# Performance work log

Hardware: AMD Instinct MI355X
Metric: run time of the kernel (lower is better)

## Reference

```python
import jax, jax.numpy as jnp
import numpy as np

EPS = 1e-12
BETA = 0.25

def normalise(x, axis=-1):
    return x * jax.lax.rsqrt(jnp.mean(x * x, axis=axis, keepdims=True) + EPS)

def setup_inputs() -> dict:
    key = jax.random.key(0)
    ks = jax.random.split(key, 4)
    N, F, D, C = 8192, 512, 64, 8192
    return {
        "z": jax.random.normal(ks[0], (N, F), dtype=jnp.float32),
        "W_in": jax.random.normal(ks[1], (F, D), dtype=jnp.float32) * (1.0 / np.sqrt(F)),
        "b_in": jnp.zeros((D,), dtype=jnp.float32),
        "codebook": jax.random.normal(ks[2], (C, D), dtype=jnp.float32),
        "W_out": jax.random.normal(ks[3], (D, F), dtype=jnp.float32) * (1.0 / np.sqrt(D)),
        "b_out": jnp.zeros((F,), dtype=jnp.float32),
    }

def reference(z, W_in, b_in, codebook, W_out, b_out):
    sg = jax.lax.stop_gradient
    # input projection: [N, F] -> [N, D]
    zp = z @ W_in + b_in
    zn = normalise(zp)                  # [N, D]
    cn = normalise(codebook)            # [C, D]
    # squared euclidean distance via matmul expansion (same math as
    # sum((z[:,None]-c[None])**2, -1), avoids [N,C,D] materialization)
    z_sq = jnp.sum(zn * zn, axis=-1, keepdims=True)          # [N, 1]
    c_sq = jnp.sum(cn * cn, axis=-1)[None, :]                # [1, C]
    distance = z_sq + c_sq - 2.0 * (zn @ cn.T)               # [N, C]
    idxes = jnp.argmin(distance, axis=-1)                    # [N]
    codes = normalise(codebook[idxes], axis=-1)               # [N, D]
    loss = BETA * jnp.mean((sg(zn) - codes) ** 2) + jnp.mean((zn - sg(codes)) ** 2)
    codes = zn + sg(codes - zn)                               # straight-through
    out = codes @ W_out + b_out                               # [N, F]
    return (out, loss, idxes)
```

## Files before the change

kernel.cpp:

```cpp
#include <hip/hip_runtime.h>
#include <hip/hip_bf16.h>

#define N_ROWS 8192
#define F_DIM  512
#define D_DIM  64
#define C_CODES 8192

typedef __attribute__((ext_vector_type(8))) short bf16x8;
typedef __attribute__((ext_vector_type(4))) float f32x4;

__device__ __forceinline__ unsigned short rne_bf16(float x) {
  unsigned u = __float_as_uint(x);
  return (unsigned short)((u + 0x7FFFu + ((u >> 16) & 1u)) >> 16);
}
__device__ __forceinline__ float bf16_to_f(unsigned short u) {
  return __uint_as_float(((unsigned)u) << 16);
}
__device__ __forceinline__ void limb3(const float* xs, bf16x8& H, bf16x8& M, bf16x8& L) {
  #pragma unroll
  for (int j = 0; j < 8; ++j) {
    float x = xs[j];
    unsigned short h = rne_bf16(x);
    float r1 = x - bf16_to_f(h);
    unsigned short m = rne_bf16(r1);
    float r2 = r1 - bf16_to_f(m);
    unsigned short lo = rne_bf16(r2);
    H[j] = (short)h; M[j] = (short)m; L[j] = (short)lo;
  }
}

typedef __attribute__((address_space(1))) const unsigned char gas_uchar;
typedef __attribute__((address_space(3))) unsigned char las_uchar;
__device__ __forceinline__ void gld_lds16(const void* g, void* l) {
  __builtin_amdgcn_global_load_lds((gas_uchar*)g, (las_uchar*)l, 16, 0, 0);
}

__global__ __launch_bounds__(256) void k_prep(
    const float* __restrict__ W_in, const float* __restrict__ W_out,
    const float* __restrict__ cb,
    unsigned short* __restrict__ win_sw, unsigned short* __restrict__ wout_sw,
    float* __restrict__ cn, unsigned short* __restrict__ cn_sw) {
  const int tid = threadIdx.x, w = tid >> 6, l = tid & 63;
  const int lo = l & 15, hi = l >> 4;
  const int bid = blockIdx.x;

  if (bid < 16) {
    const int task = bid * 4 + w;
    const int kc = task >> 2, cg = task & 3;
    float xs[8];
    #pragma unroll
    for (int j = 0; j < 8; ++j)
      xs[j] = W_in[(size_t)(kc * 32 + hi * 8 + j) * D_DIM + cg * 16 + lo];
    bf16x8 H, M, L;
    limb3(xs, H, M, L);
    const int fb = (kc * 4 + cg) * 3;
    unsigned short* d0 = win_sw + (size_t)(fb + 0) * 512 + l * 8;
    unsigned short* d1 = win_sw + (size_t)(fb + 1) * 512 + l * 8;
    unsigned short* d2 = win_sw + (size_t)(fb + 2) * 512 + l * 8;
    #pragma unroll
    for (int j = 0; j < 8; ++j) { d0[j] = (unsigned short)H[j]; d1[j] = (unsigned short)M[j]; d2[j] = (unsigned short)L[j]; }
  } else if (bid < 32) {
    const int task = (bid - 16) * 4 + w;
    const int cg = task >> 1, c = task & 1;
    float xs[8];
    #pragma unroll
    for (int j = 0; j < 8; ++j)
      xs[j] = W_out[(size_t)(c * 32 + hi * 8 + j) * F_DIM + cg * 16 + lo];
    bf16x8 H, M, L;
    limb3(xs, H, M, L);
    const int fb = (cg * 2 + c) * 3;
    unsigned short* d0 = wout_sw + (size_t)(fb + 0) * 512 + l * 8;
    unsigned short* d1 = wout_sw + (size_t)(fb + 1) * 512 + l * 8;
    unsigned short* d2 = wout_sw + (size_t)(fb + 2) * 512 + l * 8;
    #pragma unroll
    for (int j = 0; j < 8; ++j) { d0[j] = (unsigned short)H[j]; d1[j] = (unsigned short)M[j]; d2[j] = (unsigned short)L[j]; }
  } else {
    const int g = (bid - 32) * 4 + w;
    const int code = g * 16 + lo;
    float xs[2][8];
    float s = 0.0f;
    #pragma unroll
    for (int c = 0; c < 2; ++c) {
      const float* sp = cb + (size_t)code * D_DIM + c * 32 + hi * 8;
      float4 a = *(const float4*)sp, b = *(const float4*)(sp + 4);
      xs[c][0]=a.x; xs[c][1]=a.y; xs[c][2]=a.z; xs[c][3]=a.w;
      xs[c][4]=b.x; xs[c][5]=b.y; xs[c][6]=b.z; xs[c][7]=b.w;
      #pragma unroll
      for (int j = 0; j < 8; ++j) s += xs[c][j] * xs[c][j];
    }
    s += __shfl_xor(s, 16);
    s += __shfl_xor(s, 32);
    float inv = rsqrtf(s * (1.0f / 64.0f) + 1e-12f);
    #pragma unroll
    for (int c = 0; c < 2; ++c) {
      #pragma unroll
      for (int j = 0; j < 8; ++j) xs[c][j] *= inv;
      float* dp = cn + (size_t)code * D_DIM + c * 32 + hi * 8;
      *(float4*)dp = make_float4(xs[c][0], xs[c][1], xs[c][2], xs[c][3]);
      *(float4*)(dp + 4) = make_float4(xs[c][4], xs[c][5], xs[c][6], xs[c][7]);
      bf16x8 H, M, L;
      limb3(xs[c], H, M, L);
      const int fb = (g * 2 + c) * 3;
      unsigned short* d0 = cn_sw + (size_t)(fb + 0) * 512 + l * 8;
      unsigned short* d1 = cn_sw + (size_t)(fb + 1) * 512 + l * 8;
      unsigned short* d2 = cn_sw + (size_t)(fb + 2) * 512 + l * 8;
      #pragma unroll
      for (int j = 0; j < 8; ++j) { d0[j] = (unsigned short)H[j]; d1[j] = (unsigned short)M[j]; d2[j] = (unsigned short)L[j]; }
    }
  }
}

__global__ __launch_bounds__(256) void k_zn(
    const float* __restrict__ z, const unsigned short* __restrict__ w_in_sw,
    const float* __restrict__ b_in, float* __restrict__ zn,
    unsigned short* __restrict__ zn_sw) {
  __shared__ float red[4096];
  __shared__ float t_lds[16 * 65];
  const int tid = threadIdx.x, w = tid >> 6, l = tid & 63;
  const int lo = l & 15, hi = l >> 4;
  const int g = blockIdx.x;
  const int r0 = g * 16;
  const int kcb = w * 4;
  const bf16x8* Bptr = (const bf16x8*)w_in_sw;
  const float* zbase = z + (size_t)(r0 + lo) * F_DIM + hi * 8;

  f32x4 acc[4];
  #pragma unroll
  for (int cg = 0; cg < 4; ++cg) acc[cg] = (f32x4){0.f, 0.f, 0.f, 0.f};

  bf16x8 Bu[12], Bv[12];
  #pragma unroll
  for (int i = 0; i < 12; ++i) Bu[i] = Bptr[((size_t)kcb * 12 + i) * 64 + l];
  float4 za = *(const float4*)(zbase + kcb * 32);
  float4 zb = *(const float4*)(zbase + kcb * 32 + 4);

  #define ZMFMA(BCUR)                                                         \
    {                                                                         \
      float xs[8] = {za.x, za.y, za.z, za.w, zb.x, zb.y, zb.z, zb.w};         \
      bf16x8 Ah, Am, Al;                                                      \
      limb3(xs, Ah, Am, Al);                                                  \
      _Pragma("unroll")                                                       \
      for (int cg = 0; cg < 4; ++cg) {                                        \
        f32x4 t = acc[cg];                                                    \
        t = __builtin_amdgcn_mfma_f32_16x16x32_bf16(Ah, BCUR[cg*3+0], t, 0,0,0); \
        t = __builtin_amdgcn_mfma_f32_16x16x32_bf16(Ah, BCUR[cg*3+1], t, 0,0,0); \
        t = __builtin_amdgcn_mfma_f32_16x16x32_bf16(Am, BCUR[cg*3+0], t, 0,0,0); \
        t = __builtin_amdgcn_mfma_f32_16x16x32_bf16(Ah, BCUR[cg*3+2], t, 0,0,0); \
        t = __builtin_amdgcn_mfma_f32_16x16x32_bf16(Al, BCUR[cg*3+0], t, 0,0,0); \
        t = __builtin_amdgcn_mfma_f32_16x16x32_bf16(Am, BCUR[cg*3+1], t, 0,0,0); \
        acc[cg] = t;                                                          \
      }                                                                       \
    }

  {
    float4 na = *(const float4*)(zbase + (kcb + 1) * 32);
    float4 nb = *(const float4*)(zbase + (kcb + 1) * 32 + 4);
    #pragma unroll
    for (int i = 0; i < 12; ++i) Bv[i] = Bptr[((size_t)(kcb + 1) * 12 + i) * 64 + l];
    ZMFMA(Bu)
    za = na; zb = nb;
  }
  {
    float4 na = *(const float4*)(zbase + (kcb + 2) * 32);
    float4 nb = *(const float4*)(zbase + (kcb + 2) * 32 + 4);
    #pragma unroll
    for (int i = 0; i < 12; ++i) Bu[i] = Bptr[((size_t)(kcb + 2) * 12 + i) * 64 + l];
    ZMFMA(Bv)
    za = na; zb = nb;
  }
  {
    float4 na = *(const float4*)(zbase + (kcb + 3) * 32);
    float4 nb = *(const float4*)(zbase + (kcb + 3) * 32 + 4);
    #pragma unroll
    for (int i = 0; i < 12; ++i) Bv[i] = Bptr[((size_t)(kcb + 3) * 12 + i) * 64 + l];
    ZMFMA(Bu)
    za = na; zb = nb;
  }
  ZMFMA(Bv)
  #undef ZMFMA

  #pragma unroll
  for (int cg = 0; cg < 4; ++cg)
    #pragma unroll
    for (int r = 0; r < 4; ++r)
      red[((w * 4 + cg) * 4 + r) * 64 + l] = acc[cg][r];
  __syncthreads();

  {
    float v[4], s = 0.0f;
    #pragma unroll
    for (int cg = 0; cg < 4; ++cg) {
      float t = b_in[cg * 16 + lo];
      #pragma unroll
      for (int w2 = 0; w2 < 4; ++w2) t += red[((w2 * 4 + cg) * 4 + w) * 64 + l];
      v[cg] = t; s += t * t;
    }
    s += __shfl_xor(s, 1);
    s += __shfl_xor(s, 2);
    s += __shfl_xor(s, 4);
    s += __shfl_xor(s, 8);
    float inv = rsqrtf(s * (1.0f / 64.0f) + 1e-12f);
    #pragma unroll
    for (int cg = 0; cg < 4; ++cg)
      t_lds[(hi * 4 + w) * 65 + cg * 16 + lo] = v[cg] * inv;
  }
  __syncthreads();

  if (w < 2) {
    const int c = w;
    float xs[8];
    #pragma unroll
    for (int j = 0; j < 8; ++j) xs[j] = t_lds[lo * 65 + c * 32 + hi * 8 + j];
    float* dp = zn + (size_t)(r0 + lo) * D_DIM + c * 32 + hi * 8;
    *(float4*)dp = make_float4(xs[0], xs[1], xs[2], xs[3]);
    *(float4*)(dp + 4) = make_float4(xs[4], xs[5], xs[6], xs[7]);
    bf16x8 H, M, L;
    limb3(xs, H, M, L);
    const int fb = (g * 2 + c) * 3;
    unsigned short* d0 = zn_sw + (size_t)(fb + 0) * 512 + l * 8;
    unsigned short* d1 = zn_sw + (size_t)(fb + 1) * 512 + l * 8;
    unsigned short* d2 = zn_sw + (size_t)(fb + 2) * 512 + l * 8;
    #pragma unroll
    for (int j = 0; j < 8; ++j) { d0[j] = (unsigned short)H[j]; d1[j] = (unsigned short)M[j]; d2[j] = (unsigned short)L[j]; }
  }
}

__global__ __launch_bounds__(256) void k_argmax(
    const unsigned short* __restrict__ zn_sw,
    const unsigned short* __restrict__ cn_sw,
    float* __restrict__ pval, int* __restrict__ pidx) {
  __shared__ short smem[2 * 12 * 512];
  const int tid = threadIdx.x;
  const int w = tid >> 6, l = tid & 63;
  const int lo = l & 15, hi = l >> 4;
  const int gA0 = (blockIdx.x * 4 + w) * 2;
  const int gB0 = blockIdx.y * 32;
  const bf16x8* Ab = (const bf16x8*)zn_sw;
  const char* Bbytes = (const char*)cn_sw;

  bf16x8 A0[2][3], A1[2][3];
  #pragma unroll
  for (int c = 0; c < 2; ++c)
    #pragma unroll
    for (int m = 0; m < 3; ++m) {
      A0[c][m] = Ab[(size_t)((gA0 * 2 + c) * 3 + m) * 64 + l];
      A1[c][m] = Ab[(size_t)(((gA0 + 1) * 2 + c) * 3 + m) * 64 + l];
    }

  float bv[8];
  int bi[8];
  #pragma unroll
  for (int i = 0; i < 8; ++i) { bv[i] = -1e30f; bi[i] = 0; }
  int cand = blockIdx.y * 512 + lo;

  #define STAGE(b, s)                                                         \
    {                                                                         \
      const int fb = (gB0 + (s) * 2) * 6 + w * 3;                             \
      _Pragma("unroll")                                                       \
      for (int i = 0; i < 3; ++i)                                             \
        gld_lds16(Bbytes + ((size_t)(fb + i) << 10) + (size_t)l * 16,         \
                  &smem[((b) * 12 + w * 3 + i) * 512]);                       \
    }

  #define MF(A_, B_, C_) __builtin_amdgcn_mfma_f32_16x16x32_bf16(A_, B_, C_, 0, 0, 0)

  #define COMPUTE(LF)                                                         \
    {                                                                         \
      bf16x8 Bf[6];                                                           \
      _Pragma("unroll")                                                       \
      for (int i = 0; i < 6; ++i)                                             \
        Bf[i] = *(const bf16x8*)&smem[((LF) + i) * 512 + l * 8];              \
      f32x4 a0 = {0.f,0.f,0.f,0.f}, a1 = {0.f,0.f,0.f,0.f};                   \
      f32x4 a2 = {0.f,0.f,0.f,0.f}, a3 = {0.f,0.f,0.f,0.f};                   \
      a0 = MF(A0[0][0], Bf[0], a0); a1 = MF(A0[1][0], Bf[3], a1);             \
      a2 = MF(A1[0][0], Bf[0], a2); a3 = MF(A1[1][0], Bf[3], a3);             \
      a0 = MF(A0[0][0], Bf[1], a0); a1 = MF(A0[1][0], Bf[4], a1);             \
      a2 = MF(A1[0][0], Bf[1], a2); a3 = MF(A1[1][0], Bf[4], a3);             \
      a0 = MF(A0[0][1], Bf[0], a0); a1 = MF(A0[1][1], Bf[3], a1);             \
      a2 = MF(A1[0][1], Bf[0], a2); a3 = MF(A1[1][1], Bf[3], a3);             \
      a0 = MF(A0[0][0], Bf[2], a0); a1 = MF(A0[1][0], Bf[5], a1);             \
      a2 = MF(A1[0][0], Bf[2], a2); a3 = MF(A1[1][0], Bf[5], a3);             \
      a0 = MF(A0[0][2], Bf[0], a0); a1 = MF(A0[1][2], Bf[3], a1);             \
      a2 = MF(A1[0][2], Bf[0], a2); a3 = MF(A1[1][2], Bf[3], a3);             \
      a0 = MF(A0[0][1], Bf[1], a0); a1 = MF(A0[1][1], Bf[4], a1);             \
      a2 = MF(A1[0][1], Bf[1], a2); a3 = MF(A1[1][1], Bf[4], a3);             \
      _Pragma("unroll")                                                       \
      for (int r = 0; r < 4; ++r) {                                           \
        float d0 = a0[r] + a1[r];                                             \
        if (d0 > bv[r]) { bv[r] = d0; bi[r] = cand; }                         \
        float d1 = a2[r] + a3[r];                                             \
        if (d1 > bv[4 + r]) { bv[4 + r] = d1; bi[4 + r] = cand; }             \
      }                                                                       \
      cand += 16;                                                             \
    }

  STAGE(0, 0)
  __syncthreads();
  int cur = 0;
  for (int s = 0; s < 16; ++s) {
    if (s < 15) STAGE(cur ^ 1, s + 1)
    COMPUTE(cur * 12 + 0)
    COMPUTE(cur * 12 + 6)
    __syncthreads();
    cur ^= 1;
  }
  #undef STAGE
  #undef COMPUTE
  #undef MF

  #pragma unroll
  for (int i = 0; i < 8; ++i) {
    float v = bv[i]; int ix = bi[i];
    #pragma unroll
    for (int m = 1; m < 16; m <<= 1) {
      float ov = __shfl_xor(v, m);
      int oi = __shfl_xor(ix, m);
      if (ov > v || (ov == v && oi < ix)) { v = ov; ix = oi; }
    }
    bv[i] = v; bi[i] = ix;
  }
  if (lo == 0) {
    int off = blockIdx.y * N_ROWS;
    int base0 = gA0 * 16 + hi * 4;
    int base1 = (gA0 + 1) * 16 + hi * 4;
    #pragma unroll
    for (int r = 0; r < 4; ++r) {
      pval[off + base0 + r] = bv[r];     pidx[off + base0 + r] = bi[r];
      pval[off + base1 + r] = bv[4 + r]; pidx[off + base1 + r] = bi[4 + r];
    }
  }
}

__global__ __launch_bounds__(256) void k_out(
    const float* __restrict__ cn, const float* __restrict__ zn,
    const float* __restrict__ pval, const int* __restrict__ pidx,
    const unsigned short* __restrict__ w_out_sw,
    const float* __restrict__ b_out, float* __restrict__ out,
    float* __restrict__ idx_f, float* __restrict__ pl) {
  const int tid = threadIdx.x, w = tid >> 6, l = tid & 63;
  const int lo = l & 15, hi = l >> 4;
  const int r0 = blockIdx.x * 16;
  const int row = r0 + lo;

  float v = pval[row];
  int ix = pidx[row];
  #pragma unroll
  for (int q = 1; q < 16; ++q) {
    float vq = pval[q * N_ROWS + row];
    int iq = pidx[q * N_ROWS + row];
    if (vq > v) { v = vq; ix = iq; }
  }
  if (w == 0 && hi == 0) idx_f[row] = (float)ix;

  bf16x8 A[2][3];
  float lp = 0.0f;
  #pragma unroll
  for (int c = 0; c < 2; ++c) {
    const float* cp = cn + (size_t)ix * D_DIM + c * 32 + hi * 8;
    const float* zp = zn + (size_t)row * D_DIM + c * 32 + hi * 8;
    float4 c0 = *(const float4*)cp, c1 = *(const float4*)(cp + 4);
    float4 z0 = *(const float4*)zp, z1 = *(const float4*)(zp + 4);
    float xs[8] = {c0.x, c0.y, c0.z, c0.w, c1.x, c1.y, c1.z, c1.w};
    float zs[8] = {z0.x, z0.y, z0.z, z0.w, z1.x, z1.y, z1.z, z1.w};
    limb3(xs, A[c][0], A[c][1], A[c][2]);
    #pragma unroll
    for (int j = 0; j < 8; ++j) { float d = xs[j] - zs[j]; lp += d * d; }
  }
  if (w == 0) {
    #pragma unroll
    for (int m = 1; m < 64; m <<= 1) lp += __shfl_xor(lp, m);
    if (l == 0) pl[blockIdx.x] = lp;
  }

  const bf16x8* Bptr = (const bf16x8*)w_out_sw;
  const int cgb = w * 8;
  bf16x8 Bu[6], Bv[6];
  #pragma unroll
  for (int i = 0; i < 6; ++i) Bu[i] = Bptr[((size_t)cgb * 6 + i) * 64 + l];

  #define OSTEP(BCUR, BNXT, CG)                                               \
    {                                                                         \
      _Pragma("unroll")                                                       \
      for (int i = 0; i < 6; ++i)                                             \
        BNXT[i] = Bptr[((size_t)((CG) + 1) * 6 + i) * 64 + l];                \
      f32x4 a0 = {0.f,0.f,0.f,0.f}, a1 = {0.f,0.f,0.f,0.f};                   \
      a0 = __builtin_amdgcn_mfma_f32_16x16x32_bf16(A[0][0], BCUR[0], a0, 0,0,0); \
      a1 = __builtin_amdgcn_mfma_f32_16x16x32_bf16(A[1][0], BCUR[3], a1, 0,0,0); \
      a0 = __builtin_amdgcn_mfma_f32_16x16x32_bf16(A[0][0], BCUR[1], a0, 0,0,0); \
      a1 = __builtin_amdgcn_mfma_f32_16x16x32_bf16(A[1][0], BCUR[4], a1, 0,0,0); \
      a0 = __builtin_amdgcn_mfma_f32_16x16x32_bf16(A[0][1], BCUR[0], a0, 0,0,0); \
      a1 = __builtin_amdgcn_mfma_f32_16x16x32_bf16(A[1][1], BCUR[3], a1, 0,0,0); \
      a0 = __builtin_amdgcn_mfma_f32_16x16x32_bf16(A[0][0], BCUR[2], a0, 0,0,0); \
      a1 = __builtin_amdgcn_mfma_f32_16x16x32_bf16(A[1][0], BCUR[5], a1, 0,0,0); \
      a0 = __builtin_amdgcn_mfma_f32_16x16x32_bf16(A[0][2], BCUR[0], a0, 0,0,0); \
      a1 = __builtin_amdgcn_mfma_f32_16x16x32_bf16(A[1][2], BCUR[3], a1, 0,0,0); \
      a0 = __builtin_amdgcn_mfma_f32_16x16x32_bf16(A[0][1], BCUR[1], a0, 0,0,0); \
      a1 = __builtin_amdgcn_mfma_f32_16x16x32_bf16(A[1][1], BCUR[4], a1, 0,0,0); \
      float bb = b_out[(CG) * 16 + lo];                                       \
      _Pragma("unroll")                                                       \
      for (int r = 0; r < 4; ++r)                                             \
        out[(size_t)(r0 + hi * 4 + r) * F_DIM + (CG) * 16 + lo] =             \
            a0[r] + a1[r] + bb;                                               \
    }

  for (int cg = cgb; cg < cgb + 8; cg += 2) {
    OSTEP(Bu, Bv, cg)
    OSTEP(Bv, Bu, cg + 1)
  }
  #undef OSTEP
}

__global__ __launch_bounds__(64) void k_loss_final(
    const float* __restrict__ pl, float* __restrict__ loss_out) {
  const int l = threadIdx.x;
  float s = 0.0f;
  #pragma unroll
  for (int i = 0; i < 8; ++i) s += pl[l + 64 * i];
  #pragma unroll
  for (int m = 1; m < 64; m <<= 1) s += __shfl_xor(s, m);
  if (l == 0) loss_out[0] = s * (1.25f / (float)(N_ROWS * D_DIM));
}

extern "C" void kernel_launch(void* const* d_in, const int* in_sizes, int n_in,
                              void* d_out, int out_size, void* d_ws, size_t ws_size,
                              hipStream_t stream) {
  const float* z        = (const float*)d_in[0];
  const float* W_in     = (const float*)d_in[1];
  const float* b_in     = (const float*)d_in[2];
  const float* codebook = (const float*)d_in[3];
  const float* W_out    = (const float*)d_in[4];
  const float* b_out    = (const float*)d_in[5];

  float* outp   = (float*)d_out;
  float* loss_f = outp + (size_t)N_ROWS * F_DIM;
  float* idx_f  = loss_f + 1;

  float* wsf = (float*)d_ws;
  float* zn_ws = wsf;
  float* cn_ws = wsf + 524288;
  unsigned short* zn_sw = (unsigned short*)(wsf + 1048576);
  unsigned short* cn_sw = (unsigned short*)(wsf + 1835008);
  unsigned short* win_sw  = (unsigned short*)(wsf + 2625536);
  unsigned short* wout_sw = (unsigned short*)(wsf + 2674688);
  float* pval_ws = wsf + 2723840;
  int*   pidx_ws = (int*)(wsf + 2854912);
  float* pl_ws   = wsf + 2985984;

  hipLaunchKernelGGL(k_prep, dim3(160), dim3(256), 0, stream,
                     W_in, W_out, codebook, win_sw, wout_sw, cn_ws, cn_sw);
  hipLaunchKernelGGL(k_zn, dim3(512), dim3(256), 0, stream,
                     z, win_sw, b_in, zn_ws, zn_sw);
  hipLaunchKernelGGL(k_argmax, dim3(64, 16), dim3(256), 0, stream,
                     zn_sw, cn_sw, pval_ws, pidx_ws);
  hipLaunchKernelGGL(k_out, dim3(512), dim3(256), 0, stream,
                     cn_ws, zn_ws, pval_ws, pidx_ws, wout_sw, b_out,
                     outp, idx_f, pl_ws);
  hipLaunchKernelGGL(k_loss_final, dim3(1), dim3(64), 0, stream,
                     pl_ws, loss_f);
}
```

Before: 141.6 us.

## Switch argmax GEMM to 32x32x16 MFMA with matching swizzled operand layout

```diff
diff --git a/kernel.cpp b/kernel.cpp
--- a/kernel.cpp
+++ b/kernel.cpp
@@ -8,6 +8,7 @@
 
 typedef __attribute__((ext_vector_type(8))) short bf16x8;
 typedef __attribute__((ext_vector_type(4))) float f32x4;
+typedef __attribute__((ext_vector_type(16))) float f32x16;
 
 __device__ __forceinline__ unsigned short rne_bf16(float x) {
   unsigned u = __float_as_uint(x);
@@ -55,10 +56,9 @@
     limb3(xs, H, M, L);
     const int fb = (kc * 4 + cg) * 3;
     unsigned short* d0 = win_sw + (size_t)(fb + 0) * 512 + l * 8;
-    unsigned short* d1 = win_sw + (size_t)(fb + 1) * 512 + l * 8;
-    unsigned short* d2 = win_sw + (size_t)(fb + 2) * 512 + l * 8;
-    #pragma unroll
-    for (int j = 0; j < 8; ++j) { d0[j] = (unsigned short)H[j]; d1[j] = (unsigned short)M[j]; d2[j] = (unsigned short)L[j]; }
+    *(bf16x8*)d0 = H;
+    *(bf16x8*)(d0 + 512) = M;
+    *(bf16x8*)(d0 + 1024) = L;
   } else if (bid < 32) {
     const int task = (bid - 16) * 4 + w;
     const int cg = task >> 1, c = task & 1;
@@ -70,13 +70,13 @@
     limb3(xs, H, M, L);
     const int fb = (cg * 2 + c) * 3;
     unsigned short* d0 = wout_sw + (size_t)(fb + 0) * 512 + l * 8;
-    unsigned short* d1 = wout_sw + (size_t)(fb + 1) * 512 + l * 8;
-    unsigned short* d2 = wout_sw + (size_t)(fb + 2) * 512 + l * 8;
-    #pragma unroll
-    for (int j = 0; j < 8; ++j) { d0[j] = (unsigned short)H[j]; d1[j] = (unsigned short)M[j]; d2[j] = (unsigned short)L[j]; }
+    *(bf16x8*)d0 = H;
+    *(bf16x8*)(d0 + 512) = M;
+    *(bf16x8*)(d0 + 1024) = L;
   } else {
     const int g = (bid - 32) * 4 + w;
     const int code = g * 16 + lo;
+    const int Gc = g >> 1, hgc = g & 1;
     float xs[2][8];
     float s = 0.0f;
     #pragma unroll
@@ -100,12 +100,13 @@
       *(float4*)(dp + 4) = make_float4(xs[c][4], xs[c][5], xs[c][6], xs[c][7]);
       bf16x8 H, M, L;
       limb3(xs[c], H, M, L);
-      const int fb = (g * 2 + c) * 3;
-      unsigned short* d0 = cn_sw + (size_t)(fb + 0) * 512 + l * 8;
-      unsigned short* d1 = cn_sw + (size_t)(fb + 1) * 512 + l * 8;
-      unsigned short* d2 = cn_sw + (size_t)(fb + 2) * 512 + l * 8;
-      #pragma unroll
-      for (int j = 0; j < 8; ++j) { d0[j] = (unsigned short)H[j]; d1[j] = (unsigned short)M[j]; d2[j] = (unsigned short)L[j]; }
+      const int kc = c * 2 + (hi >> 1);
+      const int lane = hgc * 16 + lo + 32 * (hi & 1);
+      unsigned short* d0 =
+          cn_sw + ((size_t)Gc * 4 + kc) * 3 * 512 + (size_t)lane * 8;
+      *(bf16x8*)d0 = H;
+      *(bf16x8*)(d0 + 512) = M;
+      *(bf16x8*)(d0 + 1024) = L;
     }
   }
 }
@@ -206,22 +207,25 @@
   }
   __syncthreads();
 
-  if (w < 2) {
-    const int c = w;
+  if (l < 32) {
+    const int r = l & 15, kh = l >> 4;
+    const int kc = w;
     float xs[8];
     #pragma unroll
-    for (int j = 0; j < 8; ++j) xs[j] = t_lds[lo * 65 + c * 32 + hi * 8 + j];
-    float* dp = zn + (size_t)(r0 + lo) * D_DIM + c * 32 + hi * 8;
+    for (int j = 0; j < 8; ++j)
+      xs[j] = t_lds[r * 65 + kc * 16 + kh * 8 + j];
+    float* dp = zn + (size_t)(r0 + r) * D_DIM + kc * 16 + kh * 8;
     *(float4*)dp = make_float4(xs[0], xs[1], xs[2], xs[3]);
     *(float4*)(dp + 4) = make_float4(xs[4], xs[5], xs[6], xs[7]);
     bf16x8 H, M, L;
     limb3(xs, H, M, L);
-    const int fb = (g * 2 + c) * 3;
-    unsigned short* d0 = zn_sw + (size_t)(fb + 0) * 512 + l * 8;
-    unsigned short* d1 = zn_sw + (size_t)(fb + 1) * 512 + l * 8;
-    unsigned short* d2 = zn_sw + (size_t)(fb + 2) * 512 + l * 8;
-    #pragma unroll
-    for (int j = 0; j < 8; ++j) { d0[j] = (unsigned short)H[j]; d1[j] = (unsigned short)M[j]; d2[j] = (unsigned short)L[j]; }
+    const int G = g >> 1, hg = g & 1;
+    const int lane = hg * 16 + r + 32 * kh;
+    unsigned short* d0 =
+        zn_sw + ((size_t)G * 4 + kc) * 3 * 512 + (size_t)lane * 8;
+    *(bf16x8*)d0 = H;
+    *(bf16x8*)(d0 + 512) = M;
+    *(bf16x8*)(d0 + 1024) = L;
   }
 }
 
@@ -232,66 +236,53 @@
   __shared__ short smem[2 * 12 * 512];
   const int tid = threadIdx.x;
   const int w = tid >> 6, l = tid & 63;
-  const int lo = l & 15, hi = l >> 4;
-  const int gA0 = (blockIdx.x * 4 + w) * 2;
-  const int gB0 = blockIdx.y * 32;
+  const int G = blockIdx.x * 4 + w;
+  const int gB0 = blockIdx.y * 16;
   const bf16x8* Ab = (const bf16x8*)zn_sw;
   const char* Bbytes = (const char*)cn_sw;
 
-  bf16x8 A0[2][3], A1[2][3];
-  #pragma unroll
-  for (int c = 0; c < 2; ++c)
-    #pragma unroll
-    for (int m = 0; m < 3; ++m) {
-      A0[c][m] = Ab[(size_t)((gA0 * 2 + c) * 3 + m) * 64 + l];
-      A1[c][m] = Ab[(size_t)(((gA0 + 1) * 2 + c) * 3 + m) * 64 + l];
-    }
-
-  float bv[8];
-  int bi[8];
-  #pragma unroll
-  for (int i = 0; i < 8; ++i) { bv[i] = -1e30f; bi[i] = 0; }
-  int cand = blockIdx.y * 512 + lo;
-
-  #define STAGE(b, s)                                                         \
-    {                                                                         \
-      const int fb = (gB0 + (s) * 2) * 6 + w * 3;                             \
-      _Pragma("unroll")                                                       \
-      for (int i = 0; i < 3; ++i)                                             \
-        gld_lds16(Bbytes + ((size_t)(fb + i) << 10) + (size_t)l * 16,         \
-                  &smem[((b) * 12 + w * 3 + i) * 512]);                       \
-    }
-
-  #define MF(A_, B_, C_) __builtin_amdgcn_mfma_f32_16x16x32_bf16(A_, B_, C_, 0, 0, 0)
-
-  #define COMPUTE(LF)                                                         \
-    {                                                                         \
-      bf16x8 Bf[6];                                                           \
-      _Pragma("unroll")                                                       \
-      for (int i = 0; i < 6; ++i)                                             \
-        Bf[i] = *(const bf16x8*)&smem[((LF) + i) * 512 + l * 8];              \
-      f32x4 a0 = {0.f,0.f,0.f,0.f}, a1 = {0.f,0.f,0.f,0.f};                   \
-      f32x4 a2 = {0.f,0.f,0.f,0.f}, a3 = {0.f,0.f,0.f,0.f};                   \
-      a0 = MF(A0[0][0], Bf[0], a0); a1 = MF(A0[1][0], Bf[3], a1);             \
-      a2 = MF(A1[0][0], Bf[0], a2); a3 = MF(A1[1][0], Bf[3], a3);             \
-      a0 = MF(A0[0][0], Bf[1], a0); a1 = MF(A0[1][0], Bf[4], a1);             \
-      a2 = MF(A1[0][0], Bf[1], a2); a3 = MF(A1[1][0], Bf[4], a3);             \
-      a0 = MF(A0[0][1], Bf[0], a0); a1 = MF(A0[1][1], Bf[3], a1);             \
-      a2 = MF(A1[0][1], Bf[0], a2); a3 = MF(A1[1][1], Bf[3], a3);             \
-      a0 = MF(A0[0][0], Bf[2], a0); a1 = MF(A0[1][0], Bf[5], a1);             \
-      a2 = MF(A1[0][0], Bf[2], a2); a3 = MF(A1[1][0], Bf[5], a3);             \
-      a0 = MF(A0[0][2], Bf[0], a0); a1 = MF(A0[1][2], Bf[3], a1);             \
-      a2 = MF(A1[0][2], Bf[0], a2); a3 = MF(A1[1][2], Bf[3], a3);             \
-      a0 = MF(A0[0][1], Bf[1], a0); a1 = MF(A0[1][1], Bf[4], a1);             \
-      a2 = MF(A1[0][1], Bf[1], a2); a3 = MF(A1[1][1], Bf[4], a3);             \
-      _Pragma("unroll")                                                       \
-      for (int r = 0; r < 4; ++r) {                                           \
-        float d0 = a0[r] + a1[r];                                             \
-        if (d0 > bv[r]) { bv[r] = d0; bi[r] = cand; }                         \
-        float d1 = a2[r] + a3[r];                                             \
-        if (d1 > bv[4 + r]) { bv[4 + r] = d1; bi[4 + r] = cand; }             \
-      }                                                                       \
-      cand += 16;                                                             \
+  bf16x8 A[4][3];
+  #pragma unroll
+  for (int kc = 0; kc < 4; ++kc)
+    #pragma unroll
+    for (int m = 0; m < 3; ++m)
+      A[kc][m] = Ab[((size_t)(G * 4 + kc) * 3 + m) * 64 + l];
+
+  float bv[16];
+  int bi[16];
+  #pragma unroll
+  for (int i = 0; i < 16; ++i) { bv[i] = -1e30f; bi[i] = 0; }
+
+  #define STAGE(b, s)                                                        \
+    {                                                                        \
+      const int fb = (gB0 + (s)) * 12 + w * 3;                               \
+      _Pragma("unroll")                                                      \
+      for (int i = 0; i < 3; ++i)                                            \
+        gld_lds16(Bbytes + ((size_t)(fb + i) << 10) + (size_t)l * 16,        \
+                  &smem[((b) * 12 + w * 3 + i) * 512]);                      \
+    }
+
+  #define MF32(A_, B_, C_) __builtin_amdgcn_mfma_f32_32x32x16_bf16(A_, B_, C_, 0, 0, 0)
+
+  #define COMPUTE(LF, s)                                                     \
+    {                                                                        \
+      f32x16 acc = {};                                                       \
+      _Pragma("unroll")                                                      \
+      for (int kc = 0; kc < 4; ++kc) {                                       \
+        bf16x8 B0 = *(const bf16x8*)&smem[((LF) + kc * 3 + 0) * 512 + l * 8];\
+        bf16x8 B1 = *(const bf16x8*)&smem[((LF) + kc * 3 + 1) * 512 + l * 8];\
+        bf16x8 B2 = *(const bf16x8*)&smem[((LF) + kc * 3 + 2) * 512 + l * 8];\
+        acc = MF32(A[kc][0], B0, acc);                                       \
+        acc = MF32(A[kc][0], B1, acc);                                       \
+        acc = MF32(A[kc][1], B0, acc);                                       \
+        acc = MF32(A[kc][0], B2, acc);                                       \
+        acc = MF32(A[kc][2], B0, acc);                                       \
+        acc = MF32(A[kc][1], B1, acc);                                       \
+      }                                                                      \
+      const int cand = blockIdx.y * 512 + (s) * 32 + (l & 31);               \
+      _Pragma("unroll")                                                      \
+      for (int r = 0; r < 16; ++r)                                           \
+        if (acc[r] > bv[r]) { bv[r] = acc[r]; bi[r] = cand; }                \
     }
 
   STAGE(0, 0)
@@ -299,34 +290,33 @@
   int cur = 0;
   for (int s = 0; s < 16; ++s) {
     if (s < 15) STAGE(cur ^ 1, s + 1)
-    COMPUTE(cur * 12 + 0)
-    COMPUTE(cur * 12 + 6)
+    COMPUTE(cur * 12, s)
     __syncthreads();
     cur ^= 1;
   }
   #undef STAGE
   #undef COMPUTE
-  #undef MF
-
-  #pragma unroll
-  for (int i = 0; i < 8; ++i) {
+  #undef MF32
+
+  #pragma unroll
+  for (int i = 0; i < 16; ++i) {
     float v = bv[i]; int ix = bi[i];
     #pragma unroll
-    for (int m = 1; m < 16; m <<= 1) {
+    for (int m = 1; m < 32; m <<= 1) {
       float ov = __shfl_xor(v, m);
       int oi = __shfl_xor(ix, m);
       if (ov > v || (ov == v && oi < ix)) { v = ov; ix = oi; }
     }
     bv[i] = v; bi[i] = ix;
   }
-  if (lo == 0) {
-    int off = blockIdx.y * N_ROWS;
-    int base0 = gA0 * 16 + hi * 4;
-    int base1 = (gA0 + 1) * 16 + hi * 4;
-    #pragma unroll
-    for (int r = 0; r < 4; ++r) {
-      pval[off + base0 + r] = bv[r];     pidx[off + base0 + r] = bi[r];
-      pval[off + base1 + r] = bv[4 + r]; pidx[off + base1 + r] = bi[4 + r];
+  if ((l & 31) == 0) {
+    const int off = blockIdx.y * N_ROWS;
+    const int rb = G * 32 + 4 * (l >> 5);
+    #pragma unroll
+    for (int r = 0; r < 16; ++r) {
+      const int row = rb + (r & 3) + 8 * (r >> 2);
+      pval[off + row] = bv[r];
+      pidx[off + row] = bi[r];
     }
   }
 }
```

After: 147.1 us. +3.9%, slower.
